# Performance work log

Hardware: AMD Instinct MI355X
Metric: run time of the kernel (lower is better)

The kernel has to match this reference:

```python
import jax, jax.numpy as jnp
import numpy as np

B, T, N = 32, 1024, 512


def gru_cell(x, h, Wih, Whh, bih, bhh):
    # PyTorch GRUCell math. Wih/Whh: [3N, N] rows ordered (r, z, n).
    gi = x @ Wih.T + bih  # [B, 3N]
    gh = h @ Whh.T + bhh  # [B, 3N]
    i_r, i_z, i_n = jnp.split(gi, 3, axis=-1)
    h_r, h_z, h_n = jnp.split(gh, 3, axis=-1)
    r = jax.nn.sigmoid(i_r + h_r)
    z = jax.nn.sigmoid(i_z + h_z)
    n = jnp.tanh(i_n + r * h_n)
    return (1.0 - z) * n + z * h


def setup_inputs() -> dict:
    key = jax.random.key(0)
    ks = jax.random.split(key, 5)
    s = 1.0 / np.sqrt(N)
    x_in = jax.random.normal(ks[0], (B, T, N), dtype=jnp.float32)
    WihF = jax.random.normal(ks[1], (3 * N, N), dtype=jnp.float32) * s
    WhhF = jax.random.normal(ks[2], (3 * N, N), dtype=jnp.float32) * s
    WihB = jax.random.normal(ks[3], (3 * N, N), dtype=jnp.float32) * s
    WhhB = jax.random.normal(ks[4], (3 * N, N), dtype=jnp.float32) * s
    zeros3N = jnp.zeros((3 * N,), dtype=jnp.float32)
    return {
        "x_in": x_in,
        "WihF": WihF, "WhhF": WhhF, "bihF": zeros3N, "bhhF": zeros3N,
        "WihB": WihB, "WhhB": WhhB, "bihB": zeros3N, "bhhB": zeros3N,
    }


def reference(x_in, WihF, WhhF, bihF, bhhF, WihB, WhhB, bihB, bhhB):
    # Forward GRU over x[:, t], backward GRU over x[:, T-1-t].
    # Per original code: h_enc[:, t] = concat(h_fr_t + x[:, t], h_bk_t + x[:, T-1-t])
    # (backward states are NOT re-reversed before writing).
    x_fwd = jnp.swapaxes(x_in, 0, 1)          # [T, B, N]
    x_bwd = x_fwd[::-1]                        # [T, B, N], x[:, T-1-t]

    h0 = jnp.zeros((x_in.shape[0], N), dtype=x_in.dtype)

    def step(carry, xs):
        h_fr, h_bk = carry
        xt, xrt = xs
        h_fr = gru_cell(xt, h_fr, WihF, WhhF, bihF, bhhF)
        h_bk = gru_cell(xrt, h_bk, WihB, WhhB, bihB, bhhB)
        out = jnp.concatenate([h_fr + xt, h_bk + xrt], axis=-1)  # [B, 2N]
        return (h_fr, h_bk), out

    _, h_enc = jax.lax.scan(step, (h0, h0), (x_fwd, x_bwd))  # [T, B, 2N]
    return jnp.swapaxes(h_enc, 0, 1)  # [B, T, 2N]
```

## Files before the change

### kernel.cpp

```cpp
#include <hip/hip_runtime.h>
#include <hip/hip_bf16.h>
#include <stdint.h>

#define TB 32
#define TT 1024
#define TN 512

typedef __attribute__((ext_vector_type(8))) short short8;
typedef __attribute__((ext_vector_type(4))) float f32x4;
typedef __attribute__((ext_vector_type(4))) short short4v;
typedef unsigned long long ull;

#define GI_OFF   262144ull
#define GI_BYTES 402653184ull

static __device__ inline unsigned short f2bf(float f) {
  union { __hip_bfloat16 h; unsigned short u; } c;
  c.h = __float2bfloat16(f);
  return c.u;
}

static __device__ inline short8 pack_bf8(const float* __restrict__ p) {
  float4 a = *(const float4*)p;
  float4 b = *(const float4*)(p + 4);
  short8 o;
  o[0] = (short)f2bf(a.x); o[1] = (short)f2bf(a.y);
  o[2] = (short)f2bf(a.z); o[3] = (short)f2bf(a.w);
  o[4] = (short)f2bf(b.x); o[5] = (short)f2bf(b.y);
  o[6] = (short)f2bf(b.z); o[7] = (short)f2bf(b.w);
  return o;
}

#define HLOAD_DEV(dst, base, imm)                                          \
  asm volatile("global_load_dwordx4 %0, %1, off offset:" #imm " sc0 sc1"   \
               : "=v"(dst) : "v"(base) : "memory")

__global__ void prep_kernel(short4v* __restrict__ hbuf, unsigned* __restrict__ flags) {
  const int i = blockIdx.x * 256 + threadIdx.x;
  if (i < (2 * 2 * TB * TN / 4)) {
    short4v z; z.x = 0; z.y = 0; z.z = 0; z.w = 0;
    hbuf[i] = z;
  }
  if (i < 128) flags[i] = 0u;
}

__global__ __launch_bounds__(256) void gi_kernel(
    const float* __restrict__ x,
    const float* __restrict__ wihF, const float* __restrict__ wihB,
    const float* __restrict__ bihF, const float* __restrict__ bihB,
    float* __restrict__ gi)
{
  const int wg   = blockIdx.x;
  const int j    = wg & 15;
  const int tc   = (wg >> 4) & 31;
  const int dir  = wg >> 9;
  const int tid  = threadIdx.x;
  const int lane = tid & 63;
  const int w    = tid >> 6;
  const int mt   = w & 1;
  const int nt   = w >> 1;
  const int l15  = lane & 15;
  const int l4   = lane >> 4;
  const int coln = j * 32 + nt * 16 + l15;
  const int brow = mt * 16 + l15;

  const float* wih = dir ? wihB : wihF;
  const float* bih = dir ? bihB : bihF;

  __shared__ unsigned short wlds[2][2][16][512];
  short8 bwih_n[16];
#pragma unroll
  for (int ks = 0; ks < 16; ++ks)
    bwih_n[ks] = pack_bf8(wih + (size_t)(2 * TN + coln) * TN + ks * 32 + l4 * 8);

  if (mt == 0) {
#pragma unroll
    for (int g = 0; g < 2; ++g)
#pragma unroll
      for (int ks = 0; ks < 16; ++ks) {
        short8 f = pack_bf8(wih + (size_t)(g * TN + coln) * TN + ks * 32 + l4 * 8);
        *(short8*)&wlds[nt][g][ks][lane * 8] = f;
      }
  }
  const float b0 = bih[coln];
  const float b1 = bih[TN + coln];
  const float b2 = bih[2 * TN + coln];
  __syncthreads();

  for (int tt = 0; tt < 32; ++tt) {
    const int t  = tc * 32 + tt;
    const int st = dir ? (TT - 1 - t) : t;
    const float* xr = x + (size_t)brow * (TT * TN) + (size_t)st * TN + l4 * 8;
    short8 af[16];
#pragma unroll
    for (int ks = 0; ks < 16; ++ks) af[ks] = pack_bf8(xr + ks * 32);

    f32x4 a0 = {b0, b0, b0, b0};
    f32x4 a1 = {b1, b1, b1, b1};
    f32x4 a2 = {b2, b2, b2, b2};
#pragma unroll
    for (int ks = 0; ks < 16; ++ks) {
      short8 f0 = *(const short8*)&wlds[nt][0][ks][lane * 8];
      a0 = __builtin_amdgcn_mfma_f32_16x16x32_bf16(af[ks], f0, a0, 0, 0, 0);
      short8 f1 = *(const short8*)&wlds[nt][1][ks][lane * 8];
      a1 = __builtin_amdgcn_mfma_f32_16x16x32_bf16(af[ks], f1, a1, 0, 0, 0);
      a2 = __builtin_amdgcn_mfma_f32_16x16x32_bf16(af[ks], bwih_n[ks], a2, 0, 0, 0);
    }
    float* gb = gi + ((((size_t)dir * TT + t) * 32 + (j * 2 + nt)) * 2 + mt) * 768
                   + (size_t)lane * 4;
    *(f32x4*)gb         = a0;
    *(f32x4*)(gb + 256) = a1;
    *(f32x4*)(gb + 512) = a2;
  }
}

__global__ __launch_bounds__(256, 1) void gru_kernel(
    const float* __restrict__ x,
    const float* __restrict__ whhF, const float* __restrict__ whhB,
    const float* __restrict__ bhhF, const float* __restrict__ bhhB,
    const float* __restrict__ gi,
    unsigned short* __restrict__ hbuf,
    unsigned* __restrict__ flags,
    float* __restrict__ out)
{
  const int wg  = blockIdx.x;
  const int tid = threadIdx.x;

  if (wg >= 32) {
    float a = 1.0001f;
    const float b = 0.99995f, c = 1.0e-7f;
    for (int it = 0; it < (1 << 20); ++it) {
#pragma unroll
      for (int k = 0; k < 64; ++k) a = __builtin_fmaf(a, b, c);
      if ((it & 127) == 0) {
        if (__hip_atomic_load(&flags[68], __ATOMIC_RELAXED,
                              __HIP_MEMORY_SCOPE_AGENT) != 0u) break;
      }
    }
    asm volatile("" :: "v"(a));
    return;
  }

  const int dir  = wg >> 4;
  const int j    = wg & 15;
  const int lane = tid & 63;
  const int w    = tid >> 6;
  const int mt   = w & 1;
  const int nt   = w >> 1;
  const int l15  = lane & 15;
  const int l4   = lane >> 4;
  const int coln = j * 32 + nt * 16 + l15;

  const float* whh = dir ? whhB : whhF;
  const float* bhh = dir ? bhhB : bhhF;

  unsigned char* hp = (unsigned char*)hbuf;
  unsigned* flg = flags + dir * 32;
  const int grp = dir * 2 + mt;
  const int p   = j * 2 + nt;

  __shared__ unsigned short whh_lds[2][2][16][512];

  short8 bwhh_r[16];
#pragma unroll
  for (int ks = 0; ks < 16; ++ks)
    bwhh_r[ks] = pack_bf8(whh + (size_t)coln * TN + ks * 32 + l4 * 8);

  if (mt == 0) {
#pragma unroll
    for (int gg = 0; gg < 2; ++gg)
#pragma unroll
      for (int ks = 0; ks < 16; ++ks) {
        short8 f = pack_bf8(whh + (size_t)((gg + 1) * TN + coln) * TN + ks * 32 + l4 * 8);
        *(short8*)&whh_lds[nt][gg][ks][lane * 8] = f;
      }
  }

  const float bhh_r   = bhh[coln];
  const float bhh_z   = bhh[TN + coln];
  const float bias_hn = bhh[2 * TN + coln];

  float hstate[4] = {0.f, 0.f, 0.f, 0.f};
  int dead = 0;

  __syncthreads();

  const int bpat = mt * 16 + l4 * 4;
  const float* gwave = gi + ((((size_t)dir * TT) * 32 + p) * 2 + mt) * 768
                         + (size_t)lane * 4;

  for (int t = 0; t < TT; ++t) {
    const int st = dir ? (TT - 1 - t) : t;

    const float* gb = gwave + (size_t)t * 49152;
    f32x4 g_r = *(const f32x4*)(gb);
    f32x4 g_z = *(const f32x4*)(gb + 256);
    f32x4 g_n = *(const f32x4*)(gb + 512);
    float xv[4];
#pragma unroll
    for (int r = 0; r < 4; ++r)
      xv[r] = x[(size_t)(bpat + r) * (TT * TN) + (size_t)st * TN + coln];

    if (t > 0 && !dead) {
      const unsigned target = (unsigned)t;
      int spins = 0;
      for (;;) {
        unsigned v1 = 0xFFFFFFFFu, v2 = 0xFFFFFFFFu;
        if (lane < 16) {
          v1 = __hip_atomic_load(&flg[lane], __ATOMIC_RELAXED,
                                 __HIP_MEMORY_SCOPE_AGENT);
          v2 = __hip_atomic_load(&flg[lane], __ATOMIC_RELAXED,
                                 __HIP_MEMORY_SCOPE_AGENT);
        }
        if (__ballot(v1 >= target) == ~0ull) break;
        if (__ballot(v2 >= target) == ~0ull) break;
        if (++spins > (1 << 20)) { dead = 1; break; }
      }
      asm volatile("" ::: "memory");
    }

    const ull gb0 = (ull)(uintptr_t)hp + ((ull)(grp * 2 + ((t + 1) & 1)) << 14)
                  + (ull)((l4 >> 1) * 512 + l15 * 32 + (l4 & 1) * 16);
    const ull gb1 = gb0 + 4096, gb2 = gb0 + 8192, gb3 = gb0 + 12288;
    short8 hf[16];
    HLOAD_DEV(hf[0],  gb0, 0); HLOAD_DEV(hf[1],  gb0, 1024); HLOAD_DEV(hf[2],  gb0, 2048); HLOAD_DEV(hf[3],  gb0, 3072);
    HLOAD_DEV(hf[4],  gb1, 0); HLOAD_DEV(hf[5],  gb1, 1024); HLOAD_DEV(hf[6],  gb1, 2048); HLOAD_DEV(hf[7],  gb1, 3072);
    HLOAD_DEV(hf[8],  gb2, 0); HLOAD_DEV(hf[9],  gb2, 1024); HLOAD_DEV(hf[10], gb2, 2048); HLOAD_DEV(hf[11], gb2, 3072);
    HLOAD_DEV(hf[12], gb3, 0); HLOAD_DEV(hf[13], gb3, 1024); HLOAD_DEV(hf[14], gb3, 2048); HLOAD_DEV(hf[15], gb3, 3072);
    asm volatile("s_waitcnt vmcnt(0)" ::: "memory");
    __builtin_amdgcn_sched_barrier(0);

    f32x4 acc_r  = g_r + bhh_r;
    f32x4 acc_z  = g_z + bhh_z;
    f32x4 acc_in = g_n;
    f32x4 acc_hn = {bias_hn, bias_hn, bias_hn, bias_hn};

#pragma unroll
    for (int ks = 0; ks < 16; ++ks) {
      acc_r = __builtin_amdgcn_mfma_f32_16x16x32_bf16(hf[ks], bwhh_r[ks], acc_r, 0, 0, 0);
      short8 bz = *(const short8*)&whh_lds[nt][0][ks][lane * 8];
      acc_z = __builtin_amdgcn_mfma_f32_16x16x32_bf16(hf[ks], bz, acc_z, 0, 0, 0);
      short8 bn = *(const short8*)&whh_lds[nt][1][ks][lane * 8];
      acc_hn = __builtin_amdgcn_mfma_f32_16x16x32_bf16(hf[ks], bn, acc_hn, 0, 0, 0);
    }

    float hout[4];
#pragma unroll
    for (int r = 0; r < 4; ++r) {
      float rg = 1.0f / (1.0f + __expf(-acc_r[r]));
      float zg = 1.0f / (1.0f + __expf(-acc_z[r]));
      float e2 = __expf(2.0f * (acc_in[r] + rg * acc_hn[r]));
      float ng = 1.0f - 2.0f / (e2 + 1.0f);
      float hnew = (1.0f - zg) * ng + zg * hstate[r];
      hstate[r] = hnew;
      hout[r] = hnew;
    }

    {
      const int src0 = (lane & 48) + (lane & 3) * 4;
      float g0[4], g1[4], g2[4], g3[4];
#pragma unroll
      for (int k = 0; k < 4; ++k) {
        g0[k] = __shfl(hout[0], src0 + k, 64);
        g1[k] = __shfl(hout[1], src0 + k, 64);
        g2[k] = __shfl(hout[2], src0 + k, 64);
        g3[k] = __shfl(hout[3], src0 + k, 64);
      }
      const int rsel = (lane >> 2) & 3;
      float vv[4];
#pragma unroll
      for (int k = 0; k < 4; ++k) {
        float lo = (rsel & 1) ? g1[k] : g0[k];
        float hi = (rsel & 1) ? g3[k] : g2[k];
        vv[k] = (rsel & 2) ? hi : lo;
      }
      unsigned d0 = (unsigned)f2bf(vv[0]) | ((unsigned)f2bf(vv[1]) << 16);
      unsigned d1 = (unsigned)f2bf(vv[2]) | ((unsigned)f2bf(vv[3]) << 16);
      ull pk = (ull)d0 | ((ull)d1 << 32);
      ull* pw = (ull*)(hp + ((size_t)(grp * 2 + (t & 1)) << 14)
                          + (size_t)p * 512 + (size_t)lane * 8);
      __hip_atomic_store(pw, pk, __ATOMIC_RELAXED, __HIP_MEMORY_SCOPE_AGENT);
    }

    asm volatile("s_waitcnt vmcnt(0)" ::: "memory");
    __syncthreads();
    if (tid == 0)
      __hip_atomic_store(&flg[j], (unsigned)(t + 1), __ATOMIC_RELAXED,
                         __HIP_MEMORY_SCOPE_AGENT);

#pragma unroll
    for (int r = 0; r < 4; ++r) {
      __builtin_nontemporal_store(hout[r] + xv[r],
          out + (size_t)(bpat + r) * (TT * 2 * TN) + (size_t)t * (2 * TN) + dir * TN + coln);
    }
  }

  if (wg == 0 && tid == 0)
    __hip_atomic_store(&flags[68], 1u, __ATOMIC_RELAXED, __HIP_MEMORY_SCOPE_AGENT);
}

__global__ __launch_bounds__(256, 1) void gru_kernel_fb(
    const float* __restrict__ x,
    const float* __restrict__ wihF, const float* __restrict__ whhF,
    const float* __restrict__ wihB, const float* __restrict__ whhB,
    const float* __restrict__ bihF, const float* __restrict__ bhhF,
    const float* __restrict__ bihB, const float* __restrict__ bhhB,
    unsigned short* __restrict__ hbuf,
    unsigned* __restrict__ flags,
    float* __restrict__ out)
{
  const int wg   = blockIdx.x;
  const int dir  = wg >> 4;
  const int j    = wg & 15;
  const int tid  = threadIdx.x;
  const int lane = tid & 63;
  const int w    = tid >> 6;
  const int mt   = w & 1;
  const int nt   = w >> 1;
  const int l15  = lane & 15;
  const int l4   = lane >> 4;
  const int coln = j * 32 + nt * 16 + l15;
  const int brow = mt * 16 + l15;

  const float* wih = dir ? wihB : wihF;
  const float* whh = dir ? whhB : whhF;
  const float* bih = dir ? bihB : bihF;
  const float* bhh = dir ? bhhB : bhhF;

  unsigned char* hp = (unsigned char*)hbuf;
  unsigned* flg = flags + dir * 32;
  const int grp = dir * 2 + mt;
  const int p   = j * 2 + nt;

  __shared__ unsigned short wih_lds[2][2][16][512];

  short8 bwhh[3][16];
#pragma unroll
  for (int g = 0; g < 3; ++g)
#pragma unroll
    for (int ks = 0; ks < 16; ++ks)
      bwhh[g][ks] = pack_bf8(whh + (size_t)(g * TN + coln) * TN + ks * 32 + l4 * 8);

  short8 bwih_n[16];
#pragma unroll
  for (int ks = 0; ks < 16; ++ks)
    bwih_n[ks] = pack_bf8(wih + (size_t)(2 * TN + coln) * TN + ks * 32 + l4 * 8);

  if (mt == 0) {
#pragma unroll
    for (int g = 0; g < 2; ++g)
#pragma unroll
      for (int ks = 0; ks < 16; ++ks) {
        short8 f = pack_bf8(wih + (size_t)(g * TN + coln) * TN + ks * 32 + l4 * 8);
        *(short8*)&wih_lds[nt][g][ks][lane * 8] = f;
      }
  }

  const float bias_r  = bih[coln] + bhh[coln];
  const float bias_z  = bih[TN + coln] + bhh[TN + coln];
  const float bias_in = bih[2 * TN + coln];
  const float bias_hn = bhh[2 * TN + coln];

  float hstate[4] = {0.f, 0.f, 0.f, 0.f};
  int dead = 0;

  __syncthreads();

  const int bpat = mt * 16 + l4 * 4;

  for (int t = 0; t < TT; ++t) {
    const int st = dir ? (TT - 1 - t) : t;

    f32x4 acc_r  = {bias_r,  bias_r,  bias_r,  bias_r};
    f32x4 acc_z  = {bias_z,  bias_z,  bias_z,  bias_z};
    f32x4 acc_in = {bias_in, bias_in, bias_in, bias_in};
    f32x4 acc_hn = {bias_hn, bias_hn, bias_hn, bias_hn};

    const float* xr = x + (size_t)brow * (TT * TN) + (size_t)st * TN + l4 * 8;
    short8 af[16];
#pragma unroll
    for (int ks = 0; ks < 16; ++ks) af[ks] = pack_bf8(xr + ks * 32);
#pragma unroll
    for (int ks = 0; ks < 16; ++ks) {
      short8 b0 = *(const short8*)&wih_lds[nt][0][ks][lane * 8];
      acc_r = __builtin_amdgcn_mfma_f32_16x16x32_bf16(af[ks], b0, acc_r, 0, 0, 0);
      short8 b1 = *(const short8*)&wih_lds[nt][1][ks][lane * 8];
      acc_z = __builtin_amdgcn_mfma_f32_16x16x32_bf16(af[ks], b1, acc_z, 0, 0, 0);
      acc_in = __builtin_amdgcn_mfma_f32_16x16x32_bf16(af[ks], bwih_n[ks], acc_in, 0, 0, 0);
    }

    float xv[4];
#pragma unroll
    for (int r = 0; r < 4; ++r)
      xv[r] = x[(size_t)(bpat + r) * (TT * TN) + (size_t)st * TN + coln];

    if (t > 0 && !dead) {
      const unsigned target = (unsigned)t;
      int spins = 0;
      for (;;) {
        unsigned v = 0xFFFFFFFFu;
        if (lane < 16)
          v = __hip_atomic_load(&flg[lane], __ATOMIC_RELAXED, __HIP_MEMORY_SCOPE_AGENT);
        if (__ballot(v >= target) == ~0ull) break;
        if (++spins > (1 << 20)) { dead = 1; break; }
      }
      asm volatile("" ::: "memory");
    }

    const ull gb0 = (ull)(uintptr_t)hp + ((ull)(grp * 2 + ((t + 1) & 1)) << 14)
                  + (ull)((l4 >> 1) * 512 + l15 * 32 + (l4 & 1) * 16);
    const ull gb1 = gb0 + 4096, gb2 = gb0 + 8192, gb3 = gb0 + 12288;
    short8 hf[16];
    HLOAD_DEV(hf[0],  gb0, 0); HLOAD_DEV(hf[1],  gb0, 1024); HLOAD_DEV(hf[2],  gb0, 2048); HLOAD_DEV(hf[3],  gb0, 3072);
    HLOAD_DEV(hf[4],  gb1, 0); HLOAD_DEV(hf[5],  gb1, 1024); HLOAD_DEV(hf[6],  gb1, 2048); HLOAD_DEV(hf[7],  gb1, 3072);
    HLOAD_DEV(hf[8],  gb2, 0); HLOAD_DEV(hf[9],  gb2, 1024); HLOAD_DEV(hf[10], gb2, 2048); HLOAD_DEV(hf[11], gb2, 3072);
    HLOAD_DEV(hf[12], gb3, 0); HLOAD_DEV(hf[13], gb3, 1024); HLOAD_DEV(hf[14], gb3, 2048); HLOAD_DEV(hf[15], gb3, 3072);
    asm volatile("s_waitcnt vmcnt(0)" ::: "memory");
    __builtin_amdgcn_sched_barrier(0);

#pragma unroll
    for (int ks = 0; ks < 16; ++ks) {
      acc_r  = __builtin_amdgcn_mfma_f32_16x16x32_bf16(hf[ks], bwhh[0][ks], acc_r, 0, 0, 0);
      acc_z  = __builtin_amdgcn_mfma_f32_16x16x32_bf16(hf[ks], bwhh[1][ks], acc_z, 0, 0, 0);
      acc_hn = __builtin_amdgcn_mfma_f32_16x16x32_bf16(hf[ks], bwhh[2][ks], acc_hn, 0, 0, 0);
    }

    float hout[4];
#pragma unroll
    for (int r = 0; r < 4; ++r) {
      float rg = 1.0f / (1.0f + __expf(-acc_r[r]));
      float zg = 1.0f / (1.0f + __expf(-acc_z[r]));
      float e2 = __expf(2.0f * (acc_in[r] + rg * acc_hn[r]));
      float ng = 1.0f - 2.0f / (e2 + 1.0f);
      float hnew = (1.0f - zg) * ng + zg * hstate[r];
      hstate[r] = hnew;
      hout[r] = hnew;
    }

    {
      const int src0 = (lane & 48) + (lane & 3) * 4;
      float g0[4], g1[4], g2[4], g3[4];
#pragma unroll
      for (int k = 0; k < 4; ++k) {
        g0[k] = __shfl(hout[0], src0 + k, 64);
        g1[k] = __shfl(hout[1], src0 + k, 64);
        g2[k] = __shfl(hout[2], src0 + k, 64);
        g3[k] = __shfl(hout[3], src0 + k, 64);
      }
      const int rsel = (lane >> 2) & 3;
      float vv[4];
#pragma unroll
      for (int k = 0; k < 4; ++k) {
        float lo = (rsel & 1) ? g1[k] : g0[k];
        float hi = (rsel & 1) ? g3[k] : g2[k];
        vv[k] = (rsel & 2) ? hi : lo;
      }
      unsigned d0 = (unsigned)f2bf(vv[0]) | ((unsigned)f2bf(vv[1]) << 16);
      unsigned d1 = (unsigned)f2bf(vv[2]) | ((unsigned)f2bf(vv[3]) << 16);
      ull pk = (ull)d0 | ((ull)d1 << 32);
      ull* pw = (ull*)(hp + ((size_t)(grp * 2 + (t & 1)) << 14)
                          + (size_t)p * 512 + (size_t)lane * 8);
      __hip_atomic_store(pw, pk, __ATOMIC_RELAXED, __HIP_MEMORY_SCOPE_AGENT);
    }

    asm volatile("s_waitcnt vmcnt(0)" ::: "memory");
    __syncthreads();
    if (tid == 0)
      __hip_atomic_store(&flg[j], (unsigned)(t + 1), __ATOMIC_RELAXED,
                         __HIP_MEMORY_SCOPE_AGENT);

#pragma unroll
    for (int r = 0; r < 4; ++r) {
      __builtin_nontemporal_store(hout[r] + xv[r],
          out + (size_t)(bpat + r) * (TT * 2 * TN) + (size_t)t * (2 * TN) + dir * TN + coln);
    }
  }
}

extern "C" void kernel_launch(void* const* d_in, const int* in_sizes, int n_in,
                              void* d_out, int out_size, void* d_ws, size_t ws_size,
                              hipStream_t stream) {
  const float* x    = (const float*)d_in[0];
  const float* WihF = (const float*)d_in[1];
  const float* WhhF = (const float*)d_in[2];
  const float* bihF = (const float*)d_in[3];
  const float* bhhF = (const float*)d_in[4];
  const float* WihB = (const float*)d_in[5];
  const float* WhhB = (const float*)d_in[6];
  const float* bihB = (const float*)d_in[7];
  const float* bhhB = (const float*)d_in[8];

  unsigned short* hbuf = (unsigned short*)d_ws;
  unsigned* flags      = (unsigned*)((char*)d_ws + (size_t)2 * 2 * TB * TN * 2);
  float* gi            = (float*)((char*)d_ws + GI_OFF);

  prep_kernel<<<64, 256, 0, stream>>>((short4v*)hbuf, flags);

  if (ws_size >= GI_OFF + GI_BYTES) {
    gi_kernel<<<1024, 256, 0, stream>>>(x, WihF, WihB, bihF, bihB, gi);
    gru_kernel<<<256, 256, 0, stream>>>(x, WhhF, WhhB, bhhF, bhhB,
                                        gi, hbuf, flags, (float*)d_out);
  } else {
    gru_kernel_fb<<<32, 256, 0, stream>>>(
        x, WihF, WhhF, WihB, WhhB,
        bihF, bhhF, bihB, bhhB,
        hbuf, flags, (float*)d_out);
  }
}
```

Before: 4.317 ms.

## Use per-wave step flags, staged h-load waits, and drop spinner blocks

Each wave now publishes its own progress flag and waits only on the 32 waves that produce its batch-half group, instead of the block-level __syncthreads plus one flag per workgroup. This removes an intra-block barrier from every time step of the recurrence. The single vmcnt(0) wait before the MFMA chain is split into four staged waits so the early k-slices can start computing while later hidden-state loads are still in flight. The 224 extra busy-spinning workgroups and their stop flag are removed, so only the 32 working blocks are launched. That frees resources, but it may change clock or power behaviour that the spinners were keeping up.

```diff
diff --git a/kernel.cpp b/kernel.cpp
--- a/kernel.cpp
+++ b/kernel.cpp
@@ -123,24 +123,8 @@
     unsigned* __restrict__ flags,
     float* __restrict__ out)
 {
-  const int wg  = blockIdx.x;
-  const int tid = threadIdx.x;
-
-  if (wg >= 32) {
-    float a = 1.0001f;
-    const float b = 0.99995f, c = 1.0e-7f;
-    for (int it = 0; it < (1 << 20); ++it) {
-#pragma unroll
-      for (int k = 0; k < 64; ++k) a = __builtin_fmaf(a, b, c);
-      if ((it & 127) == 0) {
-        if (__hip_atomic_load(&flags[68], __ATOMIC_RELAXED,
-                              __HIP_MEMORY_SCOPE_AGENT) != 0u) break;
-      }
-    }
-    asm volatile("" :: "v"(a));
-    return;
-  }
-
+  const int wg   = blockIdx.x;
+  const int tid  = threadIdx.x;
   const int dir  = wg >> 4;
   const int j    = wg & 15;
   const int lane = tid & 63;
@@ -155,8 +139,8 @@
   const float* bhh = dir ? bhhB : bhhF;
 
   unsigned char* hp = (unsigned char*)hbuf;
-  unsigned* flg = flags + dir * 32;
   const int grp = dir * 2 + mt;
+  unsigned* flg = flags + grp * 32;
   const int p   = j * 2 + nt;
 
   __shared__ unsigned short whh_lds[2][2][16][512];
@@ -205,15 +189,11 @@
       const unsigned target = (unsigned)t;
       int spins = 0;
       for (;;) {
-        unsigned v1 = 0xFFFFFFFFu, v2 = 0xFFFFFFFFu;
-        if (lane < 16) {
-          v1 = __hip_atomic_load(&flg[lane], __ATOMIC_RELAXED,
-                                 __HIP_MEMORY_SCOPE_AGENT);
-          v2 = __hip_atomic_load(&flg[lane], __ATOMIC_RELAXED,
-                                 __HIP_MEMORY_SCOPE_AGENT);
-        }
-        if (__ballot(v1 >= target) == ~0ull) break;
-        if (__ballot(v2 >= target) == ~0ull) break;
+        unsigned v = 0xFFFFFFFFu;
+        if (lane < 32)
+          v = __hip_atomic_load(&flg[lane], __ATOMIC_RELAXED,
+                                __HIP_MEMORY_SCOPE_AGENT);
+        if (__ballot(v >= target) == ~0ull) break;
         if (++spins > (1 << 20)) { dead = 1; break; }
       }
       asm volatile("" ::: "memory");
@@ -227,22 +207,35 @@
     HLOAD_DEV(hf[4],  gb1, 0); HLOAD_DEV(hf[5],  gb1, 1024); HLOAD_DEV(hf[6],  gb1, 2048); HLOAD_DEV(hf[7],  gb1, 3072);
     HLOAD_DEV(hf[8],  gb2, 0); HLOAD_DEV(hf[9],  gb2, 1024); HLOAD_DEV(hf[10], gb2, 2048); HLOAD_DEV(hf[11], gb2, 3072);
     HLOAD_DEV(hf[12], gb3, 0); HLOAD_DEV(hf[13], gb3, 1024); HLOAD_DEV(hf[14], gb3, 2048); HLOAD_DEV(hf[15], gb3, 3072);
-    asm volatile("s_waitcnt vmcnt(0)" ::: "memory");
-    __builtin_amdgcn_sched_barrier(0);
 
     f32x4 acc_r  = g_r + bhh_r;
     f32x4 acc_z  = g_z + bhh_z;
     f32x4 acc_in = g_n;
     f32x4 acc_hn = {bias_hn, bias_hn, bias_hn, bias_hn};
 
-#pragma unroll
-    for (int ks = 0; ks < 16; ++ks) {
-      acc_r = __builtin_amdgcn_mfma_f32_16x16x32_bf16(hf[ks], bwhh_r[ks], acc_r, 0, 0, 0);
-      short8 bz = *(const short8*)&whh_lds[nt][0][ks][lane * 8];
-      acc_z = __builtin_amdgcn_mfma_f32_16x16x32_bf16(hf[ks], bz, acc_z, 0, 0, 0);
-      short8 bn = *(const short8*)&whh_lds[nt][1][ks][lane * 8];
-      acc_hn = __builtin_amdgcn_mfma_f32_16x16x32_bf16(hf[ks], bn, acc_hn, 0, 0, 0);
-    }
+#define CONSUME4(K0)                                                               \
+    _Pragma("unroll")                                                              \
+    for (int ks = (K0); ks < (K0) + 4; ++ks) {                                     \
+      acc_r = __builtin_amdgcn_mfma_f32_16x16x32_bf16(hf[ks], bwhh_r[ks], acc_r, 0, 0, 0); \
+      short8 bz = *(const short8*)&whh_lds[nt][0][ks][lane * 8];                   \
+      acc_z = __builtin_amdgcn_mfma_f32_16x16x32_bf16(hf[ks], bz, acc_z, 0, 0, 0); \
+      short8 bn = *(const short8*)&whh_lds[nt][1][ks][lane * 8];                   \
+      acc_hn = __builtin_amdgcn_mfma_f32_16x16x32_bf16(hf[ks], bn, acc_hn, 0, 0, 0); \
+    }
+
+    asm volatile("s_waitcnt vmcnt(12)" ::: "memory");
+    __builtin_amdgcn_sched_barrier(0);
+    CONSUME4(0)
+    asm volatile("s_waitcnt vmcnt(8)" ::: "memory");
+    __builtin_amdgcn_sched_barrier(0);
+    CONSUME4(4)
+    asm volatile("s_waitcnt vmcnt(4)" ::: "memory");
+    __builtin_amdgcn_sched_barrier(0);
+    CONSUME4(8)
+    asm volatile("s_waitcnt vmcnt(0)" ::: "memory");
+    __builtin_amdgcn_sched_barrier(0);
+    CONSUME4(12)
+#undef CONSUME4
 
     float hout[4];
 #pragma unroll
@@ -283,9 +276,8 @@
     }
 
     asm volatile("s_waitcnt vmcnt(0)" ::: "memory");
-    __syncthreads();
-    if (tid == 0)
-      __hip_atomic_store(&flg[j], (unsigned)(t + 1), __ATOMIC_RELAXED,
+    if (lane == 0)
+      __hip_atomic_store(&flg[p], (unsigned)(t + 1), __ATOMIC_RELAXED,
                          __HIP_MEMORY_SCOPE_AGENT);
 
 #pragma unroll
@@ -294,9 +286,6 @@
           out + (size_t)(bpat + r) * (TT * 2 * TN) + (size_t)t * (2 * TN) + dir * TN + coln);
     }
   }
-
-  if (wg == 0 && tid == 0)
-    __hip_atomic_store(&flags[68], 1u, __ATOMIC_RELAXED, __HIP_MEMORY_SCOPE_AGENT);
 }
 
 __global__ __launch_bounds__(256, 1) void gru_kernel_fb(
@@ -498,8 +487,8 @@
 
   if (ws_size >= GI_OFF + GI_BYTES) {
     gi_kernel<<<1024, 256, 0, stream>>>(x, WihF, WihB, bihF, bihB, gi);
-    gru_kernel<<<256, 256, 0, stream>>>(x, WhhF, WhhB, bhhF, bhhB,
-                                        gi, hbuf, flags, (float*)d_out);
+    gru_kernel<<<32, 256, 0, stream>>>(x, WhhF, WhhB, bhhF, bhhB,
+                                       gi, hbuf, flags, (float*)d_out);
   } else {
     gru_kernel_fb<<<32, 256, 0, stream>>>(
         x, WihF, WhhF, WihB, WhhB,
```

Result: slower. 4.797 ms (+11.1%).
